# Kernel tuning notes

Hardware: AMD Instinct MI355X
Metric: run time of the kernel (lower is better)

Reference implementation:

```python
import jax, jax.numpy as jnp
import numpy as np

COPY = 4
PAD = 0
EPS = 1e-10


def setup_inputs() -> dict:
    key = jax.random.key(0)
    k1, k2, k3, k4, k5, k6 = jax.random.split(key, 6)
    B, S, H, V, SRC_V = 1024, 128, 1024, 50000, 50000
    hidden = jax.random.normal(k1, (B, H), dtype=jnp.float32)
    src = jax.random.randint(k2, (B, S), 0, SRC_V, dtype=jnp.int64)
    attn = jax.random.uniform(k3, (B, S), dtype=jnp.float32)
    W = jax.random.normal(k4, (V, H), dtype=jnp.float32) * 0.02
    b = jax.random.normal(k5, (V,), dtype=jnp.float32) * 0.02
    alignment = jax.random.randint(k6, (SRC_V,), 0, V, dtype=jnp.int64)
    return {"hidden": hidden, "src": src, "attn": attn, "W": W, "b": b, "alignment": alignment}


def reference(hidden, src, attn, W, b, alignment):
    # logits = Linear(hidden): [B, V]
    logits = jnp.einsum("bh,vh->bv", hidden, W) + b
    # zero-out (set to 1e-10) the COPY logit before softmax
    mod_logits = logits.at[:, COPY].set(1e-10)
    prob = jax.nn.softmax(mod_logits, axis=-1)                      # [B, V]
    copy = jax.nn.sigmoid(logits[:, COPY])[:, None]                 # [B, 1]
    mul_attn = attn * copy                                          # [B, S]
    prob = prob * (1.0 - copy)                                      # [B, V]
    # map source token ids to target vocab ids, then batched scatter-add
    tgt_idx = alignment[src]                                        # [B, S]
    B = prob.shape[0]
    rows = jnp.arange(B)[:, None]                                   # [B, 1]
    out_prob = prob.at[rows, tgt_idx].add(mul_attn)                 # fused batched index_add
    out_prob = out_prob.at[:, PAD].set(EPS)
    norm = out_prob.sum(axis=1, keepdims=True)
    return jnp.log(out_prob / norm + EPS)
```

## Files before the change

kernel.cpp:

```cpp
#include <hip/hip_runtime.h>

#define B_   1024
#define S_   128
#define H_   1024
#define V_   50000
#define EPSF 1e-10f

typedef float f32x4 __attribute__((ext_vector_type(4)));
typedef short s16x8 __attribute__((ext_vector_type(8)));
typedef short s16x4 __attribute__((ext_vector_type(4)));

#define OFF_WHI 0ULL
#define OFF_WLO 102400000ULL
#define OFF_AHI 204800000ULL
#define OFF_ALO 206897152ULL
#define OFF_Z   208994304ULL
#define OFF_ST  208998400ULL
#define OFF_RT  209014784ULL
#define OFF_RV  209539072ULL
#define OFF_RL  210063360ULL
#define WS_NEED 210587648ULL

__device__ __forceinline__ void gload_lds16(const void* g, void* l) {
  __builtin_amdgcn_global_load_lds(
      (const __attribute__((address_space(1))) void*)g,
      (__attribute__((address_space(3))) void*)l, 16, 0, 0);
}

__device__ __forceinline__ void split8(f32x4 a, f32x4 b, s16x8& hi, s16x8& lo) {
  float x[8] = {a[0], a[1], a[2], a[3], b[0], b[1], b[2], b[3]};
#pragma unroll
  for (int j = 0; j < 8; ++j) {
    unsigned u = __float_as_uint(x[j]);
    hi[j] = (short)(u >> 16);
    float hf = __uint_as_float(u & 0xFFFF0000u);
    float l  = x[j] - hf;
    lo[j] = (short)(__float_as_uint(l) >> 16);
  }
}

__global__ __launch_bounds__(256) void split_planes(
    const float* __restrict__ in, short* __restrict__ hi,
    short* __restrict__ lo, int n4) {
  for (int g = blockIdx.x * 256 + threadIdx.x; g < n4; g += gridDim.x * 256) {
    f32x4 x = ((const f32x4*)in)[g];
    s16x4 h, l;
#pragma unroll
    for (int j = 0; j < 4; ++j) {
      unsigned u = __float_as_uint(x[j]);
      h[j] = (short)(u >> 16);
      float hf = __uint_as_float(u & 0xFFFF0000u);
      l[j] = (short)(__float_as_uint(x[j] - hf) >> 16);
    }
    ((s16x4*)hi)[g] = h;
    ((s16x4*)lo)[g] = l;
  }
}

__global__ void zeroZ(float* Z) { Z[blockIdx.x * 256 + threadIdx.x] = 0.f; }

constexpr int NBN = (V_ + 127) / 128;

__global__ __launch_bounds__(256, 2) void gemm_ps(
    const short* __restrict__ Whi, const short* __restrict__ Wlo,
    const short* __restrict__ Ahi, const short* __restrict__ Alo,
    const float* __restrict__ bias, float* __restrict__ out,
    float* __restrict__ Z) {
  __shared__ short lds[2][4][128 * 32];

  int bid = blockIdx.x;
  int xcd = bid & 7;
  int t8  = bid >> 3;
  int mb  = t8 & 7;
  int nbg = t8 >> 3;
  int nb  = nbg * 8 + xcd;
  if (nb >= NBN) return;

  const int brow = mb * 128;
  const int bcol = nb * 128;
  const int tid  = threadIdx.x;
  const int lane = tid & 63;
  const int wid  = tid >> 6;
  const int wr   = wid >> 1;
  const int wc   = wid & 1;

  const int rt0 = wid * 16 + (lane >> 2);
  const int kc8 = (lane & 3) * 8;
  const short* pAhi = Ahi + (size_t)(brow + rt0) * H_ + kc8;
  const short* pAlo = Alo + (size_t)(brow + rt0) * H_ + kc8;
  int gv0 = bcol + rt0;        if (gv0 > V_ - 1) gv0 = V_ - 1;
  int gv1 = bcol + 64 + rt0;   if (gv1 > V_ - 1) gv1 = V_ - 1;
  const short* pBhi0 = Whi + (size_t)gv0 * H_ + kc8;
  const short* pBhi1 = Whi + (size_t)gv1 * H_ + kc8;
  const short* pBlo0 = Wlo + (size_t)gv0 * H_ + kc8;
  const short* pBlo1 = Wlo + (size_t)gv1 * H_ + kc8;

  auto stage = [&](int bufi, int k0) {
    short* base = &lds[bufi][0][0];
    gload_lds16(pAhi + k0,          base +               wid * 512);
    gload_lds16(pAhi + 65536 + k0,  base + 2048 +        wid * 512);
    gload_lds16(pAlo + k0,          base + 4096 +        wid * 512);
    gload_lds16(pAlo + 65536 + k0,  base + 4096 + 2048 + wid * 512);
    gload_lds16(pBhi0 + k0,         base + 8192 +        wid * 512);
    gload_lds16(pBhi1 + k0,         base + 8192 + 2048 + wid * 512);
    gload_lds16(pBlo0 + k0,         base + 12288 +       wid * 512);
    gload_lds16(pBlo1 + k0,         base + 12288 + 2048 + wid * 512);
  };

  const int kg  = lane >> 4;
  const int r15 = lane & 15;
  const int arow = wr * 64 + r15;
  const int brw  = wc * 64 + r15;
  const int kofs = kg * 8;

  f32x4 acc[4][4];
#pragma unroll
  for (int i = 0; i < 4; ++i)
#pragma unroll
    for (int j = 0; j < 4; ++j) acc[i][j] = (f32x4){0.f, 0.f, 0.f, 0.f};

  stage(0, 0);
  __syncthreads();
  int buf = 0;
#pragma unroll 1
  for (int t = 0; t < 32; ++t) {
    if (t < 31) stage(buf ^ 1, (t + 1) * 32);
    const short* bp = &lds[buf][0][0];
    s16x8 ah[4], al[4], bh[4], bl[4];
#pragma unroll
    for (int mi = 0; mi < 4; ++mi) {
      ah[mi] = *(const s16x8*)(bp + (arow + mi * 16) * 32 + kofs);
      al[mi] = *(const s16x8*)(bp + 4096 + (arow + mi * 16) * 32 + kofs);
    }
#pragma unroll
    for (int ni = 0; ni < 4; ++ni) {
      bh[ni] = *(const s16x8*)(bp + 8192 + (brw + ni * 16) * 32 + kofs);
      bl[ni] = *(const s16x8*)(bp + 12288 + (brw + ni * 16) * 32 + kofs);
    }
#pragma unroll
    for (int mi = 0; mi < 4; ++mi)
#pragma unroll
      for (int ni = 0; ni < 4; ++ni)
        acc[mi][ni] = __builtin_amdgcn_mfma_f32_16x16x32_bf16(ah[mi], bh[ni], acc[mi][ni], 0, 0, 0);
#pragma unroll
    for (int mi = 0; mi < 4; ++mi)
#pragma unroll
      for (int ni = 0; ni < 4; ++ni)
        acc[mi][ni] = __builtin_amdgcn_mfma_f32_16x16x32_bf16(ah[mi], bl[ni], acc[mi][ni], 0, 0, 0);
#pragma unroll
    for (int mi = 0; mi < 4; ++mi)
#pragma unroll
      for (int ni = 0; ni < 4; ++ni)
        acc[mi][ni] = __builtin_amdgcn_mfma_f32_16x16x32_bf16(al[mi], bh[ni], acc[mi][ni], 0, 0, 0);
    __syncthreads();
    buf ^= 1;
  }

  const int colbase = bcol + wc * 64 + r15;
  const int rowbase = brow + wr * 64 + ((lane >> 4) << 2);
  float bv[4];
  bool  cv[4];
#pragma unroll
  for (int ni = 0; ni < 4; ++ni) {
    int col = colbase + ni * 16;
    cv[ni] = (col < V_);
    bv[ni] = bias[cv[ni] ? col : (V_ - 1)];
  }
#pragma unroll
  for (int ni = 0; ni < 4; ++ni) {
    if (cv[ni]) {
      int col = colbase + ni * 16;
#pragma unroll
      for (int mi = 0; mi < 4; ++mi) {
        int row0 = rowbase + mi * 16;
#pragma unroll
        for (int j = 0; j < 4; ++j)
          out[(size_t)(row0 + j) * V_ + col] = acc[mi][ni][j] + bv[ni];
      }
    }
  }
#pragma unroll
  for (int mi = 0; mi < 4; ++mi) {
#pragma unroll
    for (int j = 0; j < 4; ++j) {
      float s = 0.f;
#pragma unroll
      for (int ni = 0; ni < 4; ++ni)
        if (cv[ni]) s += __expf(acc[mi][ni][j] + bv[ni]);
      s += __shfl_xor(s, 1);
      s += __shfl_xor(s, 2);
      s += __shfl_xor(s, 4);
      s += __shfl_xor(s, 8);
      if (r15 == 0) atomicAdd(&Z[rowbase + mi * 16 + j], s);
    }
  }
}

__global__ __launch_bounds__(128) void stats_k(
    const float* __restrict__ out, const float* __restrict__ attn,
    const int* __restrict__ src, const int* __restrict__ algn,
    const float* __restrict__ Z, f32x4* __restrict__ stats,
    int* __restrict__ rec_tgt, float* __restrict__ rec_val,
    float* __restrict__ rec_logit) {
  __shared__ float sVal[S_];
  __shared__ int   sTgt[S_];
  __shared__ float sRed[2];
  __shared__ float sScat0;

  const int b = blockIdx.x;
  const int tid = threadIdx.x;
  const int lane = tid & 63, wid = tid >> 6;
  const float* row = out + (size_t)b * V_;

  if (tid == 0) sScat0 = 0.f;
  const float l4 = row[4];
  const float cp = 1.f / (1.f + __expf(-l4));
  {
    int sv = src[b * S_ + tid];
    sTgt[tid] = algn[sv];
    sVal[tid] = attn[b * S_ + tid] * cp;
  }
  __syncthreads();
  int tgt = sTgt[tid];
  bool first = true;
  float total = 0.f;
  for (int s2 = 0; s2 < S_; ++s2) {
    bool eq = (sTgt[s2] == tgt);
    if (eq && s2 < tid) first = false;
    if (eq) total += sVal[s2];
  }
  int o = b * S_ + tid;
  if (first && tgt != 0) {
    rec_tgt[o]   = tgt;
    rec_val[o]   = total;
    rec_logit[o] = row[tgt];
  } else {
    rec_tgt[o] = -1;
  }
  if (first && tgt == 0) sScat0 = total;

  float sumv = sVal[tid];
#pragma unroll
  for (int off = 32; off; off >>= 1) sumv += __shfl_down(sumv, off);
  if (lane == 0) sRed[wid] = sumv;
  __syncthreads();
  if (tid == 0) {
    float sumval = sRed[0] + sRed[1];
    float Zmod   = Z[b] - __expf(l4) + __expf(EPSF);
    float p0     = __expf(row[0]) / Zmod;
    float omc    = 1.f - cp;
    float norm   = omc + sumval + EPSF - p0 * omc - sScat0;
    f32x4 st;
    st[0] = omc / (Zmod * norm);
    st[1] = __logf(EPSF / norm + EPSF);
    st[2] = 1.f / norm;
    st[3] = 0.f;
    stats[b] = st;
  }
}

__global__ __launch_bounds__(256) void transform_k(
    float* __restrict__ out, const f32x4* __restrict__ stats) {
  const int total = (B_ * (V_ / 4));
  const int gpr   = V_ / 4;
  for (int g = blockIdx.x * 256 + threadIdx.x; g < total;
       g += gridDim.x * 256) {
    int row = g / gpr;
    int cg  = g - row * gpr;
    f32x4 st = stats[row];
    f32x4 f  = ((const f32x4*)out)[g];
    int vb   = cg * 4;
    f32x4 r;
#pragma unroll
    for (int j = 0; j < 4; ++j) {
      float x = f[j];
      int v   = vb + j;
      if (v == 4) x = EPSF;
      float y = __logf(__expf(x) * st[0] + EPSF);
      if (v == 0) y = st[1];
      r[j] = y;
    }
    ((f32x4*)out)[g] = r;
  }
}

__global__ __launch_bounds__(128) void fixup_k(
    float* __restrict__ out, const f32x4* __restrict__ stats,
    const int* __restrict__ rec_tgt, const float* __restrict__ rec_val,
    const float* __restrict__ rec_logit) {
  int b = blockIdx.x, s = threadIdx.x;
  int o = b * S_ + s;
  int t = rec_tgt[o];
  if (t < 0) return;
  f32x4 st = stats[b];
  float x  = (t == 4) ? EPSF : rec_logit[o];
  out[(size_t)b * V_ + t] = __logf(__expf(x) * st[0] + st[2] * rec_val[o] + EPSF);
}

__global__ __launch_bounds__(256, 2) void gemm_fb(
    const float* __restrict__ hid, const float* __restrict__ W,
    const float* __restrict__ bias, float* __restrict__ out) {
  __shared__ float ldsA[2][128 * 32];
  __shared__ float ldsB[2][128 * 32];
  int bid = blockIdx.x;
  int xcd = bid & 7;
  int t8  = bid >> 3;
  int mb  = t8 & 7;
  int nbg = t8 >> 3;
  int nb  = nbg * 8 + xcd;
  if (nb >= NBN) return;
  const int brow = mb * 128;
  const int bcol = nb * 128;
  const int tid  = threadIdx.x;
  const int lane = tid & 63;
  const int wid  = tid >> 6;
  const int wr   = wid >> 1;
  const int wc   = wid & 1;
  const float* gA[4];
  const float* gB[4];
#pragma unroll
  for (int i = 0; i < 4; ++i) {
    int row = i * 32 + (tid >> 3);
    int g   = (tid & 7) ^ (row & 7);
    gA[i] = hid + (size_t)(brow + row) * H_ + g * 4;
    int gv = bcol + row;
    if (gv > V_ - 1) gv = V_ - 1;
    gB[i] = W + (size_t)gv * H_ + g * 4;
  }
  auto stage = [&](int bufi, int k0) {
#pragma unroll
    for (int i = 0; i < 4; ++i)
      gload_lds16(gA[i] + k0, (char*)(&ldsA[bufi][0]) + i * 4096 + wid * 1024);
#pragma unroll
    for (int i = 0; i < 4; ++i)
      gload_lds16(gB[i] + k0, (char*)(&ldsB[bufi][0]) + i * 4096 + wid * 1024);
  };
  const int kg  = lane >> 4;
  const int r15 = lane & 15;
  int offA0[4], offA1[4], offB0[4], offB1[4];
#pragma unroll
  for (int i = 0; i < 4; ++i) {
    int ra = wr * 64 + i * 16 + r15;
    int wa = ra & 7;
    offA0[i] = ra * 128 + ((((kg << 1) | 0) ^ wa) << 4);
    offA1[i] = ra * 128 + ((((kg << 1) | 1) ^ wa) << 4);
    int rb = wc * 64 + i * 16 + r15;
    int wb = rb & 7;
    offB0[i] = rb * 128 + ((((kg << 1) | 0) ^ wb) << 4);
    offB1[i] = rb * 128 + ((((kg << 1) | 1) ^ wb) << 4);
  }
  f32x4 acc[4][4];
#pragma unroll
  for (int i = 0; i < 4; ++i)
#pragma unroll
    for (int j = 0; j < 4; ++j) acc[i][j] = (f32x4){0.f, 0.f, 0.f, 0.f};
  stage(0, 0);
  __syncthreads();
  int buf = 0;
#pragma unroll 1
  for (int t = 0; t < 32; ++t) {
    if (t < 31) stage(buf ^ 1, (t + 1) * 32);
    const char* bA = (const char*)(&ldsA[buf][0]);
    const char* bB = (const char*)(&ldsB[buf][0]);
    s16x8 ah[4], al[4], bh[4], bl[4];
#pragma unroll
    for (int mi = 0; mi < 4; ++mi)
      split8(*(const f32x4*)(bA + offA0[mi]), *(const f32x4*)(bA + offA1[mi]),
             ah[mi], al[mi]);
#pragma unroll
    for (int ni = 0; ni < 4; ++ni)
      split8(*(const f32x4*)(bB + offB0[ni]), *(const f32x4*)(bB + offB1[ni]),
             bh[ni], bl[ni]);
#pragma unroll
    for (int mi = 0; mi < 4; ++mi)
#pragma unroll
      for (int ni = 0; ni < 4; ++ni) {
        acc[mi][ni] = __builtin_amdgcn_mfma_f32_16x16x32_bf16(ah[mi], bh[ni], acc[mi][ni], 0, 0, 0);
        acc[mi][ni] = __builtin_amdgcn_mfma_f32_16x16x32_bf16(ah[mi], bl[ni], acc[mi][ni], 0, 0, 0);
        acc[mi][ni] = __builtin_amdgcn_mfma_f32_16x16x32_bf16(al[mi], bh[ni], acc[mi][ni], 0, 0, 0);
      }
    __syncthreads();
    buf ^= 1;
  }
  const int colbase = bcol + wc * 64 + r15;
  const int rowbase = brow + wr * 64 + ((lane >> 4) << 2);
#pragma unroll
  for (int ni = 0; ni < 4; ++ni) {
    int col = colbase + ni * 16;
    if (col < V_) {
      float bv = bias[col];
#pragma unroll
      for (int mi = 0; mi < 4; ++mi) {
        int row0 = rowbase + mi * 16;
#pragma unroll
        for (int j = 0; j < 4; ++j)
          out[(size_t)(row0 + j) * V_ + col] = acc[mi][ni][j] + bv;
      }
    }
  }
}

__global__ __launch_bounds__(256) void row_finish(
    float* __restrict__ out, const float* __restrict__ attn,
    const int* __restrict__ src, const int* __restrict__ algn) {
  __shared__ float sRed[4];
  __shared__ float sBro[4];
  __shared__ float sSt[4];
  __shared__ float sVal[S_];
  __shared__ int   sTgt[S_];
  __shared__ int   rTgt[S_];
  __shared__ float rVal[S_];
  __shared__ float rLog[S_];
  const int b = blockIdx.x;
  const int tid = threadIdx.x;
  const int lane = tid & 63, wid = tid >> 6;
  float* row = out + (size_t)b * V_;
  float z = 0.f;
  for (int c = tid; c < V_ / 4; c += 256) {
    f32x4 f = ((const f32x4*)row)[c];
    z += __expf(f[0]) + __expf(f[1]) + __expf(f[2]) + __expf(f[3]);
  }
#pragma unroll
  for (int off = 32; off; off >>= 1) z += __shfl_down(z, off);
  if (lane == 0) sRed[wid] = z;
  if (tid == 0) sBro[2] = 0.f;
  __syncthreads();
  if (tid == 0) {
    float Zr = sRed[0] + sRed[1] + sRed[2] + sRed[3];
    float l4 = row[4];
    sBro[0] = Zr - __expf(l4) + __expf(EPSF);
    sBro[1] = 1.f / (1.f + __expf(-l4));
  }
  __syncthreads();
  const float Z = sBro[0], cp = sBro[1];
  if (tid < S_) {
    int sv = src[b * S_ + tid];
    sTgt[tid] = algn[sv];
    sVal[tid] = attn[b * S_ + tid] * cp;
  }
  __syncthreads();
  float sumv = 0.f;
  if (tid < S_) {
    int tgt = sTgt[tid];
    bool first = true;
    float total = 0.f;
    for (int s2 = 0; s2 < S_; ++s2) {
      bool eq = (sTgt[s2] == tgt);
      if (eq && s2 < tid) first = false;
      if (eq) total += sVal[s2];
    }
    if (first && tgt != 0) {
      rTgt[tid] = tgt;
      rVal[tid] = total;
      rLog[tid] = row[tgt];
    } else {
      rTgt[tid] = -1;
    }
    if (first && tgt == 0) sBro[2] = total;
    sumv = sVal[tid];
  }
#pragma unroll
  for (int off = 32; off; off >>= 1) sumv += __shfl_down(sumv, off);
  if (lane == 0) sRed[wid] = sumv;
  __syncthreads();
  if (tid == 0) {
    float sumval = sRed[0] + sRed[1] + sRed[2] + sRed[3];
    float scat0  = sBro[2];
    float p0     = __expf(row[0]) / Z;
    float omc    = 1.f - cp;
    float norm   = omc + sumval + EPSF - p0 * omc - scat0;
    sSt[0] = omc / (Z * norm);
    sSt[1] = __logf(EPSF / norm + EPSF);
    sSt[2] = 1.f / norm;
  }
  __syncthreads();
  const float st0 = sSt[0], st1 = sSt[1], invn = sSt[2];
  for (int c = tid; c < V_ / 4; c += 256) {
    f32x4 f = ((const f32x4*)row)[c];
    int vb  = c * 4;
    f32x4 r;
#pragma unroll
    for (int j = 0; j < 4; ++j) {
      float x = f[j];
      int v   = vb + j;
      if (v == 4) x = EPSF;
      float y = __logf(__expf(x) * st0 + EPSF);
      if (v == 0) y = st1;
      r[j] = y;
    }
    ((f32x4*)row)[c] = r;
  }
  __syncthreads();
  if (tid < S_) {
    int t = rTgt[tid];
    if (t >= 0) {
      float x = (t == 4) ? EPSF : rLog[tid];
      row[t] = __logf(__expf(x) * st0 + invn * rVal[tid] + EPSF);
    }
  }
}

extern "C" void kernel_launch(void* const* d_in, const int* in_sizes, int n_in,
                              void* d_out, int out_size, void* d_ws,
                              size_t ws_size, hipStream_t stream) {
  const float* hid  = (const float*)d_in[0];
  const int*   src  = (const int*)d_in[1];
  const float* attn = (const float*)d_in[2];
  const float* W    = (const float*)d_in[3];
  const float* bias = (const float*)d_in[4];
  const int*   algn = (const int*)d_in[5];
  float* out = (float*)d_out;
  (void)in_sizes; (void)n_in; (void)out_size;

  if (ws_size >= WS_NEED) {
    char* ws = (char*)d_ws;
    short* Whi = (short*)(ws + OFF_WHI);
    short* Wlo = (short*)(ws + OFF_WLO);
    short* Ahi = (short*)(ws + OFF_AHI);
    short* Alo = (short*)(ws + OFF_ALO);
    float* Z   = (float*)(ws + OFF_Z);
    f32x4* st  = (f32x4*)(ws + OFF_ST);
    int*   rt  = (int*)(ws + OFF_RT);
    float* rv  = (float*)(ws + OFF_RV);
    float* rl  = (float*)(ws + OFF_RL);

    split_planes<<<dim3(2048), dim3(256), 0, stream>>>(W, Whi, Wlo, V_ * H_ / 4);
    split_planes<<<dim3(256), dim3(256), 0, stream>>>(hid, Ahi, Alo, B_ * H_ / 4);
    zeroZ<<<dim3(4), dim3(256), 0, stream>>>(Z);
    gemm_ps<<<dim3(3136), dim3(256), 0, stream>>>(Whi, Wlo, Ahi, Alo, bias, out, Z);
    stats_k<<<dim3(B_), dim3(S_), 0, stream>>>(out, attn, src, algn, Z, st, rt, rv, rl);
    transform_k<<<dim3(2048), dim3(256), 0, stream>>>(out, st);
    fixup_k<<<dim3(B_), dim3(S_), 0, stream>>>(out, st, rt, rv, rl);
  } else {
    gemm_fb<<<dim3(3136), dim3(256), 0, stream>>>(hid, W, bias, out);
    row_finish<<<dim3(B_), dim3(256), 0, stream>>>(out, attn, src, algn);
  }
}
```

Baseline: 783.1 us.

## Enlarge split-bf16 GEMM tile to 256x256 with staged per-plane pipelining

The split-precision GEMM moves from 128x128 tiles with 4 waves to 256x256 tiles with 8 waves, each wave holding an 8x4 accumulator block. This halves the global reloads of both operand planes per output element. The K-loop is split into three phases, each loading only the plane it needs, and uses explicit vmcnt waits, raw barriers and setprio to overlap the next plane loads with the MFMAs. The row transform kernel is also recast as a 2D grid to avoid per-element division, at the cost of higher register pressure and fewer, larger blocks that may tail across CUs.

After: 958.0 us. 22.3% more time.

```diff
diff --git a/kernel.cpp b/kernel.cpp
--- a/kernel.cpp
+++ b/kernel.cpp
@@ -21,6 +21,8 @@
 #define OFF_RL  210063360ULL
 #define WS_NEED 210587648ULL
 
+#define VMCNT(n) asm volatile("s_waitcnt vmcnt(" #n ")" ::: "memory")
+
 __device__ __forceinline__ void gload_lds16(const void* g, void* l) {
   __builtin_amdgcn_global_load_lds(
       (const __attribute__((address_space(1))) void*)g,
@@ -59,105 +61,135 @@
 
 __global__ void zeroZ(float* Z) { Z[blockIdx.x * 256 + threadIdx.x] = 0.f; }
 
-constexpr int NBN = (V_ + 127) / 128;
-
-__global__ __launch_bounds__(256, 2) void gemm_ps(
+constexpr int NBT = 196;
+
+__global__ __launch_bounds__(512, 2) void gemm8(
     const short* __restrict__ Whi, const short* __restrict__ Wlo,
     const short* __restrict__ Ahi, const short* __restrict__ Alo,
     const float* __restrict__ bias, float* __restrict__ out,
     float* __restrict__ Z) {
-  __shared__ short lds[2][4][128 * 32];
+  __shared__ short lds[2][4][256 * 32];
 
   int bid = blockIdx.x;
   int xcd = bid & 7;
   int t8  = bid >> 3;
-  int mb  = t8 & 7;
-  int nbg = t8 >> 3;
+  int mb  = t8 & 3;
+  int nbg = t8 >> 2;
   int nb  = nbg * 8 + xcd;
-  if (nb >= NBN) return;
-
-  const int brow = mb * 128;
-  const int bcol = nb * 128;
+  if (nb >= NBT) return;
+
+  const int brow = mb * 256;
+  const int bcol = nb * 256;
   const int tid  = threadIdx.x;
   const int lane = tid & 63;
   const int wid  = tid >> 6;
-  const int wr   = wid >> 1;
-  const int wc   = wid & 1;
-
-  const int rt0 = wid * 16 + (lane >> 2);
-  const int kc8 = (lane & 3) * 8;
-  const short* pAhi = Ahi + (size_t)(brow + rt0) * H_ + kc8;
-  const short* pAlo = Alo + (size_t)(brow + rt0) * H_ + kc8;
-  int gv0 = bcol + rt0;        if (gv0 > V_ - 1) gv0 = V_ - 1;
-  int gv1 = bcol + 64 + rt0;   if (gv1 > V_ - 1) gv1 = V_ - 1;
-  const short* pBhi0 = Whi + (size_t)gv0 * H_ + kc8;
-  const short* pBhi1 = Whi + (size_t)gv1 * H_ + kc8;
-  const short* pBlo0 = Wlo + (size_t)gv0 * H_ + kc8;
-  const short* pBlo1 = Wlo + (size_t)gv1 * H_ + kc8;
-
-  auto stage = [&](int bufi, int k0) {
-    short* base = &lds[bufi][0][0];
-    gload_lds16(pAhi + k0,          base +               wid * 512);
-    gload_lds16(pAhi + 65536 + k0,  base + 2048 +        wid * 512);
-    gload_lds16(pAlo + k0,          base + 4096 +        wid * 512);
-    gload_lds16(pAlo + 65536 + k0,  base + 4096 + 2048 + wid * 512);
-    gload_lds16(pBhi0 + k0,         base + 8192 +        wid * 512);
-    gload_lds16(pBhi1 + k0,         base + 8192 + 2048 + wid * 512);
-    gload_lds16(pBlo0 + k0,         base + 12288 +       wid * 512);
-    gload_lds16(pBlo1 + k0,         base + 12288 + 2048 + wid * 512);
+  const int wm   = wid >> 2;
+  const int wn   = wid & 3;
+
+  const int srow = wid * 16 + (lane >> 2);
+  const int skc  = (lane & 3) * 8;
+  const short* aHi0 = Ahi + (size_t)(brow + srow) * H_ + skc;
+  const short* aHi1 = aHi0 + 128 * H_;
+  const short* aLo0 = Alo + (size_t)(brow + srow) * H_ + skc;
+  const short* aLo1 = aLo0 + 128 * H_;
+  int v0 = bcol + srow;       if (v0 > V_ - 1) v0 = V_ - 1;
+  int v1 = bcol + 128 + srow; if (v1 > V_ - 1) v1 = V_ - 1;
+  const short* bHi0 = Whi + (size_t)v0 * H_ + skc;
+  const short* bHi1 = Whi + (size_t)v1 * H_ + skc;
+  const short* bLo0 = Wlo + (size_t)v0 * H_ + skc;
+  const short* bLo1 = Wlo + (size_t)v1 * H_ + skc;
+  const int sdst = wid * 512;
+
+  auto stageU1 = [&](int bufi, int k0) {
+    gload_lds16(aHi0 + k0, &lds[bufi][0][0] + sdst);
+    gload_lds16(aHi1 + k0, &lds[bufi][0][4096] + sdst);
+    gload_lds16(bHi0 + k0, &lds[bufi][2][0] + sdst);
+    gload_lds16(bHi1 + k0, &lds[bufi][2][4096] + sdst);
   };
-
-  const int kg  = lane >> 4;
-  const int r15 = lane & 15;
-  const int arow = wr * 64 + r15;
-  const int brw  = wc * 64 + r15;
-  const int kofs = kg * 8;
-
-  f32x4 acc[4][4];
-#pragma unroll
-  for (int i = 0; i < 4; ++i)
+  auto stageU2 = [&](int bufi, int k0) {
+    gload_lds16(bLo0 + k0, &lds[bufi][3][0] + sdst);
+    gload_lds16(bLo1 + k0, &lds[bufi][3][4096] + sdst);
+  };
+  auto stageU3 = [&](int bufi, int k0) {
+    gload_lds16(aLo0 + k0, &lds[bufi][1][0] + sdst);
+    gload_lds16(aLo1 + k0, &lds[bufi][1][4096] + sdst);
+  };
+
+  const int kg   = lane >> 4;
+  const int r15  = lane & 15;
+  const int aoff = (wm * 128 + r15) * 32 + kg * 8;
+  const int boff = (wn * 64 + r15) * 32 + kg * 8;
+
+  f32x4 acc[8][4];
+#pragma unroll
+  for (int i = 0; i < 8; ++i)
 #pragma unroll
     for (int j = 0; j < 4; ++j) acc[i][j] = (f32x4){0.f, 0.f, 0.f, 0.f};
 
-  stage(0, 0);
-  __syncthreads();
+  stageU1(0, 0);
+  stageU2(0, 0);
+  stageU3(0, 0);
+  VMCNT(4);
+  __builtin_amdgcn_s_barrier();
+
   int buf = 0;
 #pragma unroll 1
   for (int t = 0; t < 32; ++t) {
-    if (t < 31) stage(buf ^ 1, (t + 1) * 32);
-    const short* bp = &lds[buf][0][0];
-    s16x8 ah[4], al[4], bh[4], bl[4];
-#pragma unroll
-    for (int mi = 0; mi < 4; ++mi) {
-      ah[mi] = *(const s16x8*)(bp + (arow + mi * 16) * 32 + kofs);
-      al[mi] = *(const s16x8*)(bp + 4096 + (arow + mi * 16) * 32 + kofs);
-    }
-#pragma unroll
-    for (int ni = 0; ni < 4; ++ni) {
-      bh[ni] = *(const s16x8*)(bp + 8192 + (brw + ni * 16) * 32 + kofs);
-      bl[ni] = *(const s16x8*)(bp + 12288 + (brw + ni * 16) * 32 + kofs);
-    }
-#pragma unroll
-    for (int mi = 0; mi < 4; ++mi)
+    const int k0n  = (t + 1) * 32;
+    const bool more = (t < 31);
+    const short* P0 = &lds[buf][0][0];
+    const short* P1p = &lds[buf][1][0];
+    const short* P2p = &lds[buf][2][0];
+    const short* P3p = &lds[buf][3][0];
+    s16x8 a[8], bh[4], bl[4];
+
+    if (more) stageU1(buf ^ 1, k0n);
+#pragma unroll
+    for (int mi = 0; mi < 8; ++mi) a[mi] = *(const s16x8*)(P0 + aoff + mi * 512);
+#pragma unroll
+    for (int ni = 0; ni < 4; ++ni) bh[ni] = *(const s16x8*)(P2p + boff + ni * 512);
+    __builtin_amdgcn_s_setprio(1);
+#pragma unroll
+    for (int mi = 0; mi < 8; ++mi)
 #pragma unroll
       for (int ni = 0; ni < 4; ++ni)
-        acc[mi][ni] = __builtin_amdgcn_mfma_f32_16x16x32_bf16(ah[mi], bh[ni], acc[mi][ni], 0, 0, 0);
-#pragma unroll
-    for (int mi = 0; mi < 4; ++mi)
+        acc[mi][ni] = __builtin_amdgcn_mfma_f32_16x16x32_bf16(a[mi], bh[ni], acc[mi][ni], 0, 0, 0);
+    __builtin_amdgcn_s_setprio(0);
+    if (more) { VMCNT(6); } else { VMCNT(2); }
+    __builtin_amdgcn_s_barrier();
+
+    if (more) stageU2(buf ^ 1, k0n);
+#pragma unroll
+    for (int ni = 0; ni < 4; ++ni) bl[ni] = *(const s16x8*)(P3p + boff + ni * 512);
+    __builtin_amdgcn_s_setprio(1);
+#pragma unroll
+    for (int mi = 0; mi < 8; ++mi)
 #pragma unroll
       for (int ni = 0; ni < 4; ++ni)
-        acc[mi][ni] = __builtin_amdgcn_mfma_f32_16x16x32_bf16(ah[mi], bl[ni], acc[mi][ni], 0, 0, 0);
-#pragma unroll
-    for (int mi = 0; mi < 4; ++mi)
+        acc[mi][ni] = __builtin_amdgcn_mfma_f32_16x16x32_bf16(a[mi], bl[ni], acc[mi][ni], 0, 0, 0);
+    __builtin_amdgcn_s_setprio(0);
+    if (more) { VMCNT(6); } else { VMCNT(0); }
+    __builtin_amdgcn_s_barrier();
+
+    if (more) stageU3(buf ^ 1, k0n);
+#pragma unroll
+    for (int mi = 0; mi < 8; ++mi) a[mi] = *(const s16x8*)(P1p + aoff + mi * 512);
+    __builtin_amdgcn_s_setprio(1);
+#pragma unroll
+    for (int mi = 0; mi < 8; ++mi)
 #pragma unroll
       for (int ni = 0; ni < 4; ++ni)
-        acc[mi][ni] = __builtin_amdgcn_mfma_f32_16x16x32_bf16(al[mi], bh[ni], acc[mi][ni], 0, 0, 0);
-    __syncthreads();
+        acc[mi][ni] = __builtin_amdgcn_mfma_f32_16x16x32_bf16(a[mi], bh[ni], acc[mi][ni], 0, 0, 0);
+    __builtin_amdgcn_s_setprio(0);
+    if (more) {
+      VMCNT(4);
+      __builtin_amdgcn_s_barrier();
+    }
     buf ^= 1;
   }
 
-  const int colbase = bcol + wc * 64 + r15;
-  const int rowbase = brow + wr * 64 + ((lane >> 4) << 2);
+  const int colbase = bcol + wn * 64 + r15;
+  const int rowbase = brow + wm * 128 + (kg << 2);
   float bv[4];
   bool  cv[4];
 #pragma unroll
@@ -171,7 +203,7 @@
     if (cv[ni]) {
       int col = colbase + ni * 16;
 #pragma unroll
-      for (int mi = 0; mi < 4; ++mi) {
+      for (int mi = 0; mi < 8; ++mi) {
         int row0 = rowbase + mi * 16;
 #pragma unroll
         for (int j = 0; j < 4; ++j)
@@ -180,7 +212,7 @@
     }
   }
 #pragma unroll
-  for (int mi = 0; mi < 4; ++mi) {
+  for (int mi = 0; mi < 8; ++mi) {
 #pragma unroll
     for (int j = 0; j < 4; ++j) {
       float s = 0.f;
@@ -259,28 +291,30 @@
   }
 }
 
-__global__ __launch_bounds__(256) void transform_k(
+__global__ __launch_bounds__(256) void transform2(
     float* __restrict__ out, const f32x4* __restrict__ stats) {
-  const int total = (B_ * (V_ / 4));
-  const int gpr   = V_ / 4;
-  for (int g = blockIdx.x * 256 + threadIdx.x; g < total;
-       g += gridDim.x * 256) {
-    int row = g / gpr;
-    int cg  = g - row * gpr;
-    f32x4 st = stats[row];
-    f32x4 f  = ((const f32x4*)out)[g];
-    int vb   = cg * 4;
-    f32x4 r;
-#pragma unroll
-    for (int j = 0; j < 4; ++j) {
-      float x = f[j];
-      int v   = vb + j;
-      if (v == 4) x = EPSF;
-      float y = __logf(__expf(x) * st[0] + EPSF);
-      if (v == 0) y = st[1];
-      r[j] = y;
-    }
-    ((f32x4*)out)[g] = r;
+  const int b = blockIdx.y;
+  f32x4 st = stats[b];
+  float* row = out + (size_t)b * V_;
+  int cg0 = blockIdx.x * 512 + threadIdx.x;
+#pragma unroll
+  for (int rep = 0; rep < 2; ++rep) {
+    int cg = cg0 + rep * 256;
+    if (cg < V_ / 4) {
+      f32x4 f = ((const f32x4*)row)[cg];
+      int vb  = cg * 4;
+      f32x4 r;
+#pragma unroll
+      for (int j = 0; j < 4; ++j) {
+        float x = f[j];
+        int v   = vb + j;
+        if (v == 4) x = EPSF;
+        float y = __logf(__expf(x) * st[0] + EPSF);
+        if (v == 0) y = st[1];
+        r[j] = y;
+      }
+      ((f32x4*)row)[cg] = r;
+    }
   }
 }
 
@@ -308,7 +342,7 @@
   int mb  = t8 & 7;
   int nbg = t8 >> 3;
   int nb  = nbg * 8 + xcd;
-  if (nb >= NBN) return;
+  if (nb >= 391) return;
   const int brow = mb * 128;
   const int bcol = nb * 128;
   const int tid  = threadIdx.x;
@@ -527,9 +561,9 @@
     split_planes<<<dim3(2048), dim3(256), 0, stream>>>(W, Whi, Wlo, V_ * H_ / 4);
     split_planes<<<dim3(256), dim3(256), 0, stream>>>(hid, Ahi, Alo, B_ * H_ / 4);
     zeroZ<<<dim3(4), dim3(256), 0, stream>>>(Z);
-    gemm_ps<<<dim3(3136), dim3(256), 0, stream>>>(Whi, Wlo, Ahi, Alo, bias, out, Z);
+    gemm8<<<dim3(800), dim3(512), 0, stream>>>(Whi, Wlo, Ahi, Alo, bias, out, Z);
     stats_k<<<dim3(B_), dim3(S_), 0, stream>>>(out, attn, src, algn, Z, st, rt, rv, rl);
-    transform_k<<<dim3(2048), dim3(256), 0, stream>>>(out, st);
+    transform2<<<dim3(25, B_), dim3(256), 0, stream>>>(out, st);
     fixup_k<<<dim3(B_), dim3(S_), 0, stream>>>(out, st, rt, rv, rl);
   } else {
     gemm_fb<<<dim3(3136), dim3(256), 0, stream>>>(hid, W, bias, out);
```
